# Performance work log

Hardware: AMD Instinct MI355X
Metric: run time of the kernel (lower is better)

The kernel has to match this reference:

```python
import jax, jax.numpy as jnp
import numpy as np

D_MODEL = 1024
NUM_HEADS = 16
D_K = D_MODEL // NUM_HEADS


def setup_inputs() -> dict:
    key = jax.random.key(0)
    ks = jax.random.split(key, 7)
    B, S = 2, 2048
    query = jax.random.normal(ks[0], (B, S, D_MODEL), dtype=jnp.float32)
    key_t = jax.random.normal(ks[1], (B, S, D_MODEL), dtype=jnp.float32)
    value = jax.random.normal(ks[2], (B, S, D_MODEL), dtype=jnp.float32)
    attention_mask = jnp.ones((B, S), dtype=jnp.int32)
    # xavier_uniform for square d_model x d_model: limit = sqrt(6/(fan_in+fan_out))
    limit = np.sqrt(6.0 / (D_MODEL + D_MODEL)).astype(np.float32)
    def xav(k):
        return jax.random.uniform(k, (D_MODEL, D_MODEL), dtype=jnp.float32, minval=-limit, maxval=limit)
    return {
        "query": query, "key": key_t, "value": value,
        "attention_mask": attention_mask,
        "w_q": xav(ks[3]), "w_k": xav(ks[4]), "w_v": xav(ks[5]), "w_o": xav(ks[6]),
    }


def reference(query, key, value, attention_mask, w_q, w_k, w_v, w_o):
    B, S, _ = query.shape
    # torch Linear: x @ W.T  (weights stored [out, in])
    def proj(x, w):
        y = jnp.einsum('bsd,ed->bse', x, w)
        return y.reshape(B, S, NUM_HEADS, D_K).transpose(0, 2, 1, 3)  # [B,H,S,Dk]
    q = proj(query, w_q)
    k = proj(key, w_k)
    v = proj(value, w_v)
    scores = jnp.einsum('bhqd,bhkd->bhqk', q, k) / jnp.sqrt(jnp.float32(D_K))
    # mask [B,S] -> [B,1,1,S]; masked_fill where mask == 0
    mask = (attention_mask[:, None, None, :] == 0)
    scores = jnp.where(mask, jnp.float32(-1e9), scores)
    attn = jax.nn.softmax(scores, axis=-1)
    # dropout p=0.0 (eval) -> identity
    context = jnp.einsum('bhqk,bhkd->bhqd', attn, v)
    context = context.transpose(0, 2, 1, 3).reshape(B, S, D_MODEL)
    return jnp.einsum('bsd,ed->bse', context, w_o)
```

## Files before the change

kernel.cpp:

```cpp
#include <hip/hip_runtime.h>
#include <hip/hip_bf16.h>


typedef short short8  __attribute__((ext_vector_type(8)));
typedef short short4v __attribute__((ext_vector_type(4)));
typedef float f32x4   __attribute__((ext_vector_type(4)));
typedef unsigned int uint4v __attribute__((ext_vector_type(4)));

#define D_MODEL 1024
#define SEQ     2048
#define NHEAD   16
#define DKD     64
#define HSTR    (SEQ * DKD)
#define QSCALE  0.1803368801111204f
#define EXP2F(x) exp2f(x)

#define MFMA16(a, b, c) __builtin_amdgcn_mfma_f32_16x16x32_bf16((a), (b), (c), 0, 0, 0)

__device__ __forceinline__ ushort f2bf(float f) {
    union { float f; unsigned u; } a; a.f = f;
    unsigned r = a.u + 0x7fffu + ((a.u >> 16) & 1u);
    return (ushort)(r >> 16);
}
__device__ __forceinline__ unsigned cvtpk(float lo, float hi) {
    unsigned r;
    asm("v_cvt_pk_bf16_f32 %0, %1, %2" : "=v"(r) : "v"(lo), "v"(hi));
    return r;
}
union U16 { uint4v u; short8 s; };

__device__ __forceinline__ short8 frag128(const ushort* base, int row, int c0) {
    int cb = (c0 * 2) ^ ((row & 7) << 4);
    return *(const short8*)((const char*)base + row * 128 + cb);
}
__device__ __forceinline__ short8 frag256(const ushort* base, int row, int c0) {
    int cb = (c0 * 2) ^ ((row & 7) << 4);
    return *(const short8*)((const char*)base + row * 256 + cb);
}

__global__ __launch_bounds__(256) void cvt_w(
    const float* __restrict__ s0, const float* __restrict__ s1, const float* __restrict__ s2,
    ushort* __restrict__ dst)
{
    const int z = blockIdx.y;
    const float* s = (z == 0) ? s0 : ((z == 1) ? s1 : s2);
    ushort* d = dst + (size_t)z * 1048576;
    const int i = (blockIdx.x * 256 + threadIdx.x) * 8;
    f32x4 a = *(const f32x4*)(s + i);
    f32x4 b = *(const f32x4*)(s + i + 4);
    short8 o;
    #pragma unroll
    for (int u = 0; u < 4; ++u) { o[u] = (short)f2bf(a[u]); o[4 + u] = (short)f2bf(b[u]); }
    *(short8*)(d + i) = o;
}

template<int LAYOUT, int A_BF16>
__global__ __launch_bounds__(256, 3) void gemm_nt(
    const void* __restrict__ A0, const void* __restrict__ A1, const void* __restrict__ A2,
    const ushort* __restrict__ W0, const ushort* __restrict__ W1, const ushort* __restrict__ W2,
    void* __restrict__ O0, void* __restrict__ O1, void* __restrict__ O2)
{
    const int z = blockIdx.z;
    const void*   A = (z == 0) ? A0 : ((z == 1) ? A1 : A2);
    const ushort* W = (z == 0) ? W0 : ((z == 1) ? W1 : W2);
    void* O         = (z == 0) ? O0 : ((z == 1) ? O1 : O2);

    const int bm = blockIdx.x * 128;
    const int bn = blockIdx.y * 128;
    const int tid = threadIdx.x;
    const int w = tid >> 6, l = tid & 63;
    const int wr = w >> 1, wc = w & 1;

    __shared__ ushort sm[16384];

    f32x4 acc[4][4] = {};
    short8 areg[4], wreg[4];
    const int srow = tid >> 3;
    const int sc8  = (tid & 7) << 3;
    const int scb  = (sc8 * 2);

    #define GLOADT(t_) {                                                                    \
        _Pragma("unroll")                                                                   \
        for (int i = 0; i < 4; ++i) {                                                       \
            int row = i * 32 + srow;                                                        \
            if (A_BF16) {                                                                   \
                areg[i] = *(const short8*)((const ushort*)A + (size_t)(bm + row) * 1024 + (t_) * 64 + sc8); \
            } else {                                                                        \
                const float* ap = (const float*)A + (size_t)(bm + row) * 1024 + (t_) * 64 + sc8; \
                f32x4 x0 = *(const f32x4*)ap, x1 = *(const f32x4*)(ap + 4);                 \
                _Pragma("unroll")                                                           \
                for (int u = 0; u < 4; ++u) { areg[i][u] = (short)f2bf(x0[u]); areg[i][4 + u] = (short)f2bf(x1[u]); } \
            }                                                                               \
            wreg[i] = *(const short8*)(W + (size_t)(bn + row) * 1024 + (t_) * 64 + sc8);    \
        } }

    #define GWRITET() {                                                                     \
        _Pragma("unroll")                                                                   \
        for (int i = 0; i < 4; ++i) {                                                       \
            int row = i * 32 + srow;                                                        \
            int cb  = scb ^ ((row & 7) << 4);                                               \
            *(short8*)((char*)sm + row * 128 + cb) = areg[i];                               \
            *(short8*)((char*)(sm + 8192) + row * 128 + cb) = wreg[i];                      \
        } }

    GLOADT(0);
    #pragma unroll 1
    for (int t = 0; t < 16; ++t) {
        GWRITET();
        __syncthreads();
        if (t < 15) GLOADT(t + 1);

        #pragma unroll
        for (int kk = 0; kk < 2; ++kk) {
            const int c0 = kk * 32 + ((l >> 4) << 3);
            short8 af[4], bf[4];
            #pragma unroll
            for (int mi = 0; mi < 4; ++mi)
                af[mi] = frag128(sm, wr * 64 + mi * 16 + (l & 15), c0);
            #pragma unroll
            for (int ni = 0; ni < 4; ++ni)
                bf[ni] = frag128(sm + 8192, wc * 64 + ni * 16 + (l & 15), c0);
            #pragma unroll
            for (int mi = 0; mi < 4; ++mi)
                #pragma unroll
                for (int ni = 0; ni < 4; ++ni)
                    acc[mi][ni] = MFMA16(af[mi], bf[ni], acc[mi][ni]);
        }
        __syncthreads();
    }
    #undef GLOADT
    #undef GWRITET

    if (LAYOUT == 0 && z == 2) {
        #pragma unroll
        for (int mi = 0; mi < 4; ++mi) {
            #pragma unroll
            for (int ni = 0; ni < 4; ++ni) {
                int n_l = wc * 64 + ni * 16 + (l & 15);
                int m0  = wr * 64 + mi * 16 + ((l >> 4) << 2);
                short4v v4;
                #pragma unroll
                for (int j = 0; j < 4; ++j) v4[j] = (short)f2bf(acc[mi][ni][j]);
                *(short4v*)((char*)sm + n_l * 256 + ((m0 * 2) ^ ((n_l & 7) << 4))) = v4;
            }
        }
        __syncthreads();
        const int row = tid >> 1, half = tid & 1;
        const int n_g = bn + row;
        const int bb  = bm >> 11;
        ushort* Op = (ushort*)O + (size_t)(bb * NHEAD + (n_g >> 6)) * HSTR
                     + (size_t)(n_g & 63) * SEQ + (bm & 2047) + half * 64;
        #pragma unroll
        for (int u = 0; u < 8; ++u) {
            short8 c = *(const short8*)((char*)sm + row * 256
                        + (((half * 64 + u * 8) * 2) ^ ((row & 7) << 4)));
            *(short8*)(Op + u * 8) = c;
        }
        return;
    }

    const float sc = (LAYOUT == 0 && z == 0) ? QSCALE : 1.0f;
    #pragma unroll
    for (int mi = 0; mi < 4; ++mi) {
        #pragma unroll
        for (int ni = 0; ni < 4; ++ni) {
            #pragma unroll
            for (int j = 0; j < 4; ++j) {
                int m = bm + wr * 64 + mi * 16 + ((l >> 4) << 2) + j;
                int n = bn + wc * 64 + ni * 16 + (l & 15);
                if (LAYOUT == 0) {
                    int b = m >> 11, s = m & 2047, h = n >> 6, dk = n & 63;
                    ((ushort*)O)[(size_t)(b * NHEAD + h) * HSTR + s * DKD + dk] = f2bf(acc[mi][ni][j] * sc);
                } else {
                    ((float*)O)[(size_t)m * 1024 + n] = acc[mi][ni][j];
                }
            }
        }
    }
}

__global__ __launch_bounds__(256, 4) void attn_fwd(
    const ushort* __restrict__ Q, const ushort* __restrict__ K, const ushort* __restrict__ Vt,
    const int* __restrict__ mask, ushort* __restrict__ ctx)
{
    const int tid = threadIdx.x;
    const int w = tid >> 6, l = tid & 63;
    const int hi = l >> 4, lo = l & 15;
    const int id  = blockIdx.x;
    const int nid = (id & 7) * 128 + (id >> 3);
    const int bh  = nid >> 5;
    const int q0  = (nid & 31) * 64;
    const int b   = bh >> 4, h = bh & 15;

    __shared__ ushort sm[16384];
    __shared__ int mflag;

    if (tid == 0) mflag = 1;
    __syncthreads();
    {
        const int4* mp = (const int4*)(mask + b * SEQ) + tid;
        int4 m0 = mp[0], m1 = mp[256];
        if (!(m0.x && m0.y && m0.z && m0.w && m1.x && m1.y && m1.z && m1.w)) mflag = 0;
    }

    const ushort* Qh = Q  + (size_t)bh * HSTR;
    const ushort* Kh = K  + (size_t)bh * HSTR;
    const ushort* Vh = Vt + (size_t)bh * HSTR;

    short8 qf[2];
    #pragma unroll
    for (int kk = 0; kk < 2; ++kk)
        qf[kk] = *(const short8*)(Qh + (size_t)(q0 + w * 16 + lo) * DKD + kk * 32 + hi * 8);

    f32x4 acc_o[4] = {};
    float m_run = -INFINITY, l_run = 0.0f;

    const int kr = tid >> 3;
    const int kc = (tid & 7) << 3;
    const int vr = tid >> 4;
    const int vkpb = (tid & 15) << 4;

    short8  kreg[4];
    short4v vreg0[4], vreg1[4];

    #define LOADT(kt_) {                                                                   \
        _Pragma("unroll")                                                                  \
        for (int i = 0; i < 4; ++i)                                                        \
            kreg[i] = *(const short8*)(Kh + (size_t)((kt_) * 128 + i * 32 + kr) * DKD + kc); \
        _Pragma("unroll")                                                                  \
        for (int i = 0; i < 4; ++i) {                                                      \
            const ushort* vp = Vh + (size_t)(i * 16 + vr) * SEQ + (kt_) * 128 + ((tid >> 2) & 3) * 32 + (tid & 3) * 4; \
            vreg0[i] = *(const short4v*)(vp);                                              \
            vreg1[i] = *(const short4v*)(vp + 16); } }

    #define WRITET() {                                                                     \
        _Pragma("unroll")                                                                  \
        for (int i = 0; i < 4; ++i) {                                                      \
            int r = i * 32 + kr;                                                           \
            *(short8*)((char*)sm + r * 128 + ((kc * 2) ^ ((r & 7) << 4))) = kreg[i]; }     \
        _Pragma("unroll")                                                                  \
        for (int i = 0; i < 4; ++i) {                                                      \
            int r = i * 16 + vr;                                                           \
            char* p = (char*)(sm + 8192) + r * 256 + (vkpb ^ ((r & 7) << 4));              \
            *(short4v*)(p)     = vreg0[i];                                                 \
            *(short4v*)(p + 8) = vreg1[i]; } }

    LOADT(0);
    __syncthreads();
    const bool allones = (mflag != 0);
    WRITET();
    __syncthreads();

    #define HALF(nb_) {                                                                    \
        f32x4* s = s4 + 4 * (nb_);                                                         \
        if (!allones) {                                                                    \
            const int* mrow = mask + b * SEQ + kt * 128 + (nb_) * 64 + hi * 4;             \
            _Pragma("unroll")                                                              \
            for (int ni = 0; ni < 4; ++ni) {                                               \
                int4 mv = *(const int4*)(mrow + ni * 16);                                  \
                s[ni][0] = mv.x ? s[ni][0] : -1e9f;                                        \
                s[ni][1] = mv.y ? s[ni][1] : -1e9f;                                        \
                s[ni][2] = mv.z ? s[ni][2] : -1e9f;                                        \
                s[ni][3] = mv.w ? s[ni][3] : -1e9f;                                        \
            }                                                                              \
        }                                                                                  \
        float t0 = fmaxf(fmaxf(s[0][0], s[0][1]), fmaxf(s[0][2], s[0][3]));                \
        float t1 = fmaxf(fmaxf(s[1][0], s[1][1]), fmaxf(s[1][2], s[1][3]));                \
        float t2 = fmaxf(fmaxf(s[2][0], s[2][1]), fmaxf(s[2][2], s[2][3]));                \
        float t3 = fmaxf(fmaxf(s[3][0], s[3][1]), fmaxf(s[3][2], s[3][3]));                \
        float t = fmaxf(fmaxf(t0, t1), fmaxf(t2, t3));                                     \
        t = fmaxf(t, __shfl_xor(t, 16));                                                   \
        t = fmaxf(t, __shfl_xor(t, 32));                                                   \
        if (__any(t > m_run)) {                                                            \
            float mnew = fmaxf(m_run, t);                                                  \
            float c = EXP2F(m_run - mnew);                                                 \
            m_run = mnew;                                                                  \
            l_run *= c;                                                                    \
            float cj[4];                                                                   \
            _Pragma("unroll")                                                              \
            for (int j = 0; j < 4; ++j) cj[j] = __shfl(c, (l & 48) | (hi * 4 + j));        \
            _Pragma("unroll")                                                              \
            for (int ni = 0; ni < 4; ++ni)                                                 \
                _Pragma("unroll")                                                          \
                for (int j = 0; j < 4; ++j) acc_o[ni][j] *= cj[j];                         \
        }                                                                                  \
        float rsA = 0.0f;                                                                  \
        _Pragma("unroll")                                                                  \
        for (int ni = 0; ni < 4; ++ni) {                                                   \
            _Pragma("unroll")                                                              \
            for (int j = 0; j < 4; ++j) s[ni][j] = EXP2F(s[ni][j] - m_run);                \
            rsA += (s[ni][0] + s[ni][1]) + (s[ni][2] + s[ni][3]);                          \
        }                                                                                  \
        rsA += __shfl_xor(rsA, 16);                                                        \
        rsA += __shfl_xor(rsA, 32);                                                        \
        l_run += rsA;                                                                      \
        short8 pa[2];                                                                      \
        _Pragma("unroll")                                                                  \
        for (int kk = 0; kk < 2; ++kk) {                                                   \
            U16 cv;                                                                        \
            cv.u[0] = cvtpk(s[2 * kk][0],     s[2 * kk][1]);                               \
            cv.u[1] = cvtpk(s[2 * kk][2],     s[2 * kk][3]);                               \
            cv.u[2] = cvtpk(s[2 * kk + 1][0], s[2 * kk + 1][1]);                           \
            cv.u[3] = cvtpk(s[2 * kk + 1][2], s[2 * kk + 1][3]);                           \
            pa[kk] = cv.s;                                                                 \
        }                                                                                  \
        __builtin_amdgcn_s_setprio(1);                                                     \
        _Pragma("unroll")                                                                  \
        for (int kk = 0; kk < 2; ++kk) {                                                   \
            const int c0 = ((nb_) * 2 + kk) * 32 + hi * 8;                                 \
            _Pragma("unroll")                                                              \
            for (int ni = 0; ni < 4; ++ni) {                                               \
                short8 vf = frag256(sm + 8192, ni * 16 + lo, c0);                          \
                acc_o[ni] = MFMA16(pa[kk], vf, acc_o[ni]);                                 \
            }                                                                              \
        }                                                                                  \
        __builtin_amdgcn_s_setprio(0); }

    #pragma unroll 1
    for (int kt = 0; kt < 16; ++kt) {
        f32x4 s4[8] = {};
        __builtin_amdgcn_s_setprio(1);
        #pragma unroll
        for (int kk = 0; kk < 2; ++kk) {
            const int c0 = kk * 32 + hi * 8;
            #pragma unroll
            for (int ni = 0; ni < 8; ++ni) {
                short8 kf = frag128(sm, ni * 16 + lo, c0);
                s4[ni] = MFMA16(kf, qf[kk], s4[ni]);
            }
        }
        __builtin_amdgcn_s_setprio(0);

        if (kt < 15) LOADT(kt + 1);

        HALF(0)
        HALF(1)

        __syncthreads();
        if (kt < 15) {
            WRITET();
            __syncthreads();
        }
    }
    #undef HALF
    #undef LOADT
    #undef WRITET

    float inv = 1.0f / l_run;
    float invj[4];
    #pragma unroll
    for (int j = 0; j < 4; ++j)
        invj[j] = __shfl(inv, (l & 48) | (hi * 4 + j));
    #pragma unroll
    for (int ni = 0; ni < 4; ++ni)
        #pragma unroll
        for (int j = 0; j < 4; ++j) {
            int qg = q0 + w * 16 + hi * 4 + j;
            ctx[(size_t)(b * SEQ + qg) * D_MODEL + h * DKD + ni * 16 + lo] = f2bf(acc_o[ni][j] * invj[j]);
        }
}

__global__ void ws_sentinel(float* __restrict__ out, int n, float code) {
    int i = blockIdx.x * blockDim.x + threadIdx.x;
    if (i < n) out[i] = (i == 0) ? code : 0.0f;
}

extern "C" void kernel_launch(void* const* d_in, const int* in_sizes, int n_in,
                              void* d_out, int out_size, void* d_ws, size_t ws_size,
                              hipStream_t stream) {
    const float* q    = (const float*)d_in[0];
    const float* k    = (const float*)d_in[1];
    const float* v    = (const float*)d_in[2];
    const int*   mask = (const int*)d_in[3];
    const float* wq   = (const float*)d_in[4];
    const float* wk   = (const float*)d_in[5];
    const float* wv   = (const float*)d_in[6];
    const float* wo   = (const float*)d_in[7];
    float* out = (float*)d_out;

    if (ws_size < (size_t)33554432) {
        float code = 100.0f + (float)(ws_size >> 20);
        ws_sentinel<<<(out_size + 255) / 256, 256, 0, stream>>>(out, out_size, code);
        return;
    }

    ushort* ws = (ushort*)d_ws;
    ushort* Qb = ws;
    ushort* Kb = ws + 4194304;
    ushort* Vb = ws + 8388608;
    ushort* Cb = ws + 12582912;

    dim3 blk(256, 1, 1);
    cvt_w<<<dim3(512, 3), blk, 0, stream>>>(wq, wk, wv, Cb);
    gemm_nt<0, 0><<<dim3(32, 8, 3), blk, 0, stream>>>(
        q, k, v, Cb, Cb + 1048576, Cb + 2097152, Qb, Kb, Vb);
    attn_fwd<<<dim3(1024, 1, 1), blk, 0, stream>>>(Qb, Kb, Vb, mask, Cb);
    cvt_w<<<dim3(512, 1), blk, 0, stream>>>(wo, wo, wo, Qb);
    gemm_nt<1, 1><<<dim3(32, 8, 1), blk, 0, stream>>>(
        Cb, Cb, Cb, Qb, Qb, Qb, out, out, out);
}
```

Baseline: 148.5 us.

## Double-buffer K/V tiles in attention with 128-query blocks and lazy rescaling

The attention kernel now uses 512-thread blocks that each cover 128 queries, which halves the grid and lets each loaded K/V tile serve twice as many queries. The K/V tiles are double-buffered in LDS: the next tile is written to the spare buffer partway through the softmax, so one barrier per iteration is removed. The online softmax only rescales when the running max would grow by more than 8 in log2 space, which skips most rescale passes. The trade-off is 64KB of LDS per block, which likely limits occupancy, and P values before normalization can reach up to 2^8.

```diff
diff --git a/kernel.cpp b/kernel.cpp
--- a/kernel.cpp
+++ b/kernel.cpp
@@ -179,7 +179,7 @@
     }
 }
 
-__global__ __launch_bounds__(256, 4) void attn_fwd(
+__global__ __launch_bounds__(512, 4) void attn_fwd(
     const ushort* __restrict__ Q, const ushort* __restrict__ K, const ushort* __restrict__ Vt,
     const int* __restrict__ mask, ushort* __restrict__ ctx)
 {
@@ -187,20 +187,19 @@
     const int w = tid >> 6, l = tid & 63;
     const int hi = l >> 4, lo = l & 15;
     const int id  = blockIdx.x;
-    const int nid = (id & 7) * 128 + (id >> 3);
-    const int bh  = nid >> 5;
-    const int q0  = (nid & 31) * 64;
+    const int nid = (id & 7) * 64 + (id >> 3);
+    const int bh  = nid >> 4;
+    const int q0  = (nid & 15) * 128;
     const int b   = bh >> 4, h = bh & 15;
 
-    __shared__ ushort sm[16384];
+    __shared__ ushort sm[2][16384];
     __shared__ int mflag;
 
     if (tid == 0) mflag = 1;
     __syncthreads();
     {
-        const int4* mp = (const int4*)(mask + b * SEQ) + tid;
-        int4 m0 = mp[0], m1 = mp[256];
-        if (!(m0.x && m0.y && m0.z && m0.w && m1.x && m1.y && m1.z && m1.w)) mflag = 0;
+        int4 m0 = ((const int4*)(mask + b * SEQ))[tid];
+        if (!(m0.x && m0.y && m0.z && m0.w)) mflag = 0;
     }
 
     const ushort* Qh = Q  + (size_t)bh * HSTR;
@@ -220,36 +219,35 @@
     const int vr = tid >> 4;
     const int vkpb = (tid & 15) << 4;
 
-    short8  kreg[4];
-    short4v vreg0[4], vreg1[4];
+    short8  kreg[2];
+    short4v vreg0[2], vreg1[2];
 
     #define LOADT(kt_) {                                                                   \
         _Pragma("unroll")                                                                  \
-        for (int i = 0; i < 4; ++i)                                                        \
-            kreg[i] = *(const short8*)(Kh + (size_t)((kt_) * 128 + i * 32 + kr) * DKD + kc); \
-        _Pragma("unroll")                                                                  \
-        for (int i = 0; i < 4; ++i) {                                                      \
-            const ushort* vp = Vh + (size_t)(i * 16 + vr) * SEQ + (kt_) * 128 + ((tid >> 2) & 3) * 32 + (tid & 3) * 4; \
+        for (int i = 0; i < 2; ++i)                                                        \
+            kreg[i] = *(const short8*)(Kh + (size_t)((kt_) * 128 + i * 64 + kr) * DKD + kc); \
+        _Pragma("unroll")                                                                  \
+        for (int i = 0; i < 2; ++i) {                                                      \
+            const ushort* vp = Vh + (size_t)(i * 32 + vr) * SEQ + (kt_) * 128 + ((tid >> 2) & 3) * 32 + (tid & 3) * 4; \
             vreg0[i] = *(const short4v*)(vp);                                              \
             vreg1[i] = *(const short4v*)(vp + 16); } }
 
-    #define WRITET() {                                                                     \
-        _Pragma("unroll")                                                                  \
-        for (int i = 0; i < 4; ++i) {                                                      \
-            int r = i * 32 + kr;                                                           \
-            *(short8*)((char*)sm + r * 128 + ((kc * 2) ^ ((r & 7) << 4))) = kreg[i]; }     \
-        _Pragma("unroll")                                                                  \
-        for (int i = 0; i < 4; ++i) {                                                      \
-            int r = i * 16 + vr;                                                           \
-            char* p = (char*)(sm + 8192) + r * 256 + (vkpb ^ ((r & 7) << 4));              \
+    #define WRITET(buf_) {                                                                 \
+        _Pragma("unroll")                                                                  \
+        for (int i = 0; i < 2; ++i) {                                                      \
+            int r = i * 64 + kr;                                                           \
+            *(short8*)((char*)sm[buf_] + r * 128 + ((kc * 2) ^ ((r & 7) << 4))) = kreg[i]; } \
+        _Pragma("unroll")                                                                  \
+        for (int i = 0; i < 2; ++i) {                                                      \
+            int r = i * 32 + vr;                                                           \
+            char* p = (char*)(sm[buf_] + 8192) + r * 256 + (vkpb ^ ((r & 7) << 4));        \
             *(short4v*)(p)     = vreg0[i];                                                 \
             *(short4v*)(p + 8) = vreg1[i]; } }
 
-    LOADT(0);
+    LOADT(0); WRITET(0);
     __syncthreads();
     const bool allones = (mflag != 0);
-    WRITET();
-    __syncthreads();
+    const f32x4 zf = {};
 
     #define HALF(nb_) {                                                                    \
         f32x4* s = s4 + 4 * (nb_);                                                         \
@@ -271,7 +269,7 @@
         float t = fmaxf(fmaxf(t0, t1), fmaxf(t2, t3));                                     \
         t = fmaxf(t, __shfl_xor(t, 16));                                                   \
         t = fmaxf(t, __shfl_xor(t, 32));                                                   \
-        if (__any(t > m_run)) {                                                            \
+        if (!__all(t <= m_run + 8.0f)) {       \
             float mnew = fmaxf(m_run, t);                                                  \
             float c = EXP2F(m_run - mnew);                                                 \
             m_run = mnew;                                                                  \
@@ -310,7 +308,7 @@
             const int c0 = ((nb_) * 2 + kk) * 32 + hi * 8;                                 \
             _Pragma("unroll")                                                              \
             for (int ni = 0; ni < 4; ++ni) {                                               \
-                short8 vf = frag256(sm + 8192, ni * 16 + lo, c0);                          \
+                short8 vf = frag256(vb, ni * 16 + lo, c0);                                 \
                 acc_o[ni] = MFMA16(pa[kk], vf, acc_o[ni]);                                 \
             }                                                                              \
         }                                                                                  \
@@ -318,29 +316,27 @@
 
     #pragma unroll 1
     for (int kt = 0; kt < 16; ++kt) {
-        f32x4 s4[8] = {};
+        const int cur = kt & 1;
+        const ushort* kb = sm[cur];
+        const ushort* vb = sm[cur] + 8192;
+
+        if (kt < 15) LOADT(kt + 1);
+
+        f32x4 s4[8];
         __builtin_amdgcn_s_setprio(1);
         #pragma unroll
-        for (int kk = 0; kk < 2; ++kk) {
-            const int c0 = kk * 32 + hi * 8;
-            #pragma unroll
-            for (int ni = 0; ni < 8; ++ni) {
-                short8 kf = frag128(sm, ni * 16 + lo, c0);
-                s4[ni] = MFMA16(kf, qf[kk], s4[ni]);
-            }
-        }
+        for (int ni = 0; ni < 8; ++ni)
+            s4[ni] = MFMA16(frag128(kb, ni * 16 + lo, hi * 8), qf[0], zf);
+        #pragma unroll
+        for (int ni = 0; ni < 8; ++ni)
+            s4[ni] = MFMA16(frag128(kb, ni * 16 + lo, 32 + hi * 8), qf[1], s4[ni]);
         __builtin_amdgcn_s_setprio(0);
 
-        if (kt < 15) LOADT(kt + 1);
-
         HALF(0)
+        if (kt < 15) WRITET(cur ^ 1);
         HALF(1)
 
         __syncthreads();
-        if (kt < 15) {
-            WRITET();
-            __syncthreads();
-        }
     }
     #undef HALF
     #undef LOADT
@@ -394,7 +390,7 @@
     cvt_w<<<dim3(512, 3), blk, 0, stream>>>(wq, wk, wv, Cb);
     gemm_nt<0, 0><<<dim3(32, 8, 3), blk, 0, stream>>>(
         q, k, v, Cb, Cb + 1048576, Cb + 2097152, Qb, Kb, Vb);
-    attn_fwd<<<dim3(1024, 1, 1), blk, 0, stream>>>(Qb, Kb, Vb, mask, Cb);
+    attn_fwd<<<dim3(512, 1, 1), dim3(512, 1, 1), 0, stream>>>(Qb, Kb, Vb, mask, Cb);
     cvt_w<<<dim3(512, 1), blk, 0, stream>>>(wo, wo, wo, Qb);
     gemm_nt<1, 1><<<dim3(32, 8, 1), blk, 0, stream>>>(
         Cb, Cb, Cb, Qb, Qb, Qb, out, out, out);
```

After: 135.5 us. -8.7%, faster.
